# Optimization experiments

Hardware: AMD Instinct MI355X
Metric: run time of the kernel (lower is better)

Reference implementation:

```python
import jax, jax.numpy as jnp
import numpy as np


def gcn_conv(x, W, b, src, dst, n_nodes):
    """PyG GCNConv: linear transform, add self-loops, symmetric deg^-1/2 norm, scatter-add, bias."""
    h = x @ W  # [N, out] transform first (out_dim <= in_dim keeps gather traffic low)
    loop = jnp.arange(n_nodes)
    s = jnp.concatenate([src, loop])  # sources incl. self-loops
    d = jnp.concatenate([dst, loop])  # targets incl. self-loops
    deg = jnp.zeros((n_nodes,), h.dtype).at[d].add(jnp.ones((), h.dtype))
    dinv = jax.lax.rsqrt(deg)  # deg >= 1 because of self-loops
    coef = (dinv[s] * dinv[d])[:, None]  # [E+N, 1]
    out = jax.ops.segment_sum(h[s] * coef, d, num_segments=n_nodes)
    return out + b


def setup_inputs() -> dict:
    key = jax.random.key(0)
    k1, k2, k3, k4 = jax.random.split(key, 4)
    N, E = 100000, 1600000
    IN, HID, OUT = 128, 64, 32
    x = jax.random.normal(k1, (N, IN), dtype=jnp.float32)
    edge_index = jax.random.randint(k2, (2, E), 0, N, dtype=jnp.int64)
    W1 = jax.random.normal(k3, (IN, HID), dtype=jnp.float32) * (1.0 / np.sqrt(IN))
    b1 = jnp.zeros((HID,), jnp.float32)
    W2 = jax.random.normal(k4, (HID, OUT), dtype=jnp.float32) * (1.0 / np.sqrt(HID))
    b2 = jnp.zeros((OUT,), jnp.float32)
    return {"x": x, "edge_index": edge_index, "W1": W1, "b1": b1, "W2": W2, "b2": b2}


def reference(x, edge_index, W1, b1, W2, b2):
    src, dst = edge_index[0], edge_index[1]
    n = x.shape[0]
    h = jax.nn.relu(gcn_conv(x, W1, b1, src, dst, n))
    return gcn_conv(h, W2, b2, src, dst, n)
```

## Files before the change

### kernel.cpp

```cpp
#include <hip/hip_runtime.h>
#include <hip/hip_bf16.h>


#define IN_DIM 128
#define HID_DIM 64
#define OUT_DIM 32
#define BSHIFT 8
#define BSIZE 256
#define BMASK 255
#define PEB 8192
#define PTHREADS 512
#define CAPSHIFT 13

typedef __attribute__((ext_vector_type(2))) float v2f;
typedef __attribute__((ext_vector_type(8))) short short8v;
typedef __attribute__((ext_vector_type(4))) float float4v;

__device__ inline unsigned pack_bf16x2(float a, float b) {
    unsigned ua = __float_as_uint(a), ub = __float_as_uint(b);
    unsigned ra = (ua + 0x7fffu + ((ua >> 16) & 1u)) >> 16;
    unsigned rb = (ub + 0x7fffu + ((ub >> 16) & 1u)) & 0xffff0000u;
    return (ra & 0xffffu) | rb;
}
__device__ inline unsigned short f2bf(float f) {
    unsigned u = __float_as_uint(f);
    return (unsigned short)((u + 0x7fffu + ((u >> 16) & 1u)) >> 16);
}
#define BF_LO(w) __uint_as_float((w) << 16)
#define BF_HI(w) __uint_as_float((w) & 0xffff0000u)

__device__ inline v2f bfpair(unsigned u) {
    v2f r;
    r.x = __uint_as_float(u << 16);
    r.y = __uint_as_float(u & 0xffff0000u);
    return r;
}
__device__ inline void accp(v2f& a, unsigned u, float dv) {
    a.x += BF_LO(u) * dv;
    a.y += BF_HI(u) * dv;
}

#define ACC8(q)                                         \
    do {                                                \
        acc[0] += BF_LO((q).x); acc[1] += BF_HI((q).x); \
        acc[2] += BF_LO((q).y); acc[3] += BF_HI((q).y); \
        acc[4] += BF_LO((q).z); acc[5] += BF_HI((q).z); \
        acc[6] += BF_LO((q).w); acc[7] += BF_HI((q).w); \
    } while (0)

__global__ __launch_bounds__(PTHREADS) void k_part_gemm1(
        const int* __restrict__ src, const int* __restrict__ dst, int E,
        int* __restrict__ bfill, unsigned* __restrict__ packed, int B, int nPB,
        const float* __restrict__ x, const float* __restrict__ W,
        unsigned* __restrict__ g1b, int N) {
    __shared__ int cnt[512];
    __shared__ int off[512];
    __shared__ unsigned xs[32 * 66];
    int t = threadIdx.x;

    if (blockIdx.x < nPB) {
        if (t < 512) cnt[t] = 0;
        __syncthreads();
        int base = blockIdx.x * PEB;
        int dv[PEB / PTHREADS];
#pragma unroll
        for (int i = 0; i < PEB / PTHREADS; ++i) {
            int e = base + i * PTHREADS + t;
            dv[i] = (e < E) ? dst[e] : -1;
            if (dv[i] >= 0) atomicAdd(&cnt[dv[i] >> BSHIFT], 1);
        }
        __syncthreads();
        for (int b = t; b < B; b += PTHREADS) {
            int c = cnt[b];
            int o = c ? atomicAdd(&bfill[b], c) : 0;
            off[b] = (b << CAPSHIFT) + o;
        }
        __syncthreads();
#pragma unroll
        for (int i = 0; i < PEB / PTHREADS; ++i) {
            int e = base + i * PTHREADS + t;
            int d = dv[i];
            if (d >= 0) {
                int s = src[e];
                int slot = atomicAdd(&off[d >> BSHIFT], 1);
                packed[slot] = ((unsigned)s << BSHIFT) | (unsigned)(d & BMASK);
            }
        }
    } else {
        int row0 = (blockIdx.x - nPB) * 32;
        int w = t >> 6, lane = t & 63;
        int rg = w >> 2, wv = w & 3;
        int quad = lane >> 4, m = lane & 15;
        int ncol = wv * 16 + m;

        union { unsigned u[4]; short8v s; } bf[4];
#pragma unroll
        for (int kt = 0; kt < 4; ++kt) {
#pragma unroll
            for (int jp = 0; jp < 4; ++jp) {
                int k0 = kt * 32 + quad * 8 + jp * 2;
                float f0 = W[(size_t)k0 * HID_DIM + ncol];
                float f1 = W[(size_t)(k0 + 1) * HID_DIM + ncol];
                bf[kt].u[jp] = pack_bf16x2(f0, f1);
            }
        }

#pragma unroll
        for (int i = 0; i < 2; ++i) {
            int idx = t + 512 * i;
            int r = idx >> 5, c4 = idx & 31;
            int grow = row0 + r;
            float4 f = make_float4(0.f, 0.f, 0.f, 0.f);
            if (grow < N) f = ((const float4*)x)[(size_t)grow * 32 + c4];
            xs[r * 66 + c4 * 2]     = pack_bf16x2(f.x, f.y);
            xs[r * 66 + c4 * 2 + 1] = pack_bf16x2(f.z, f.w);
        }
        __syncthreads();

        float4v acc = {0.f, 0.f, 0.f, 0.f};
#pragma unroll
        for (int kt = 0; kt < 4; ++kt) {
            union { unsigned u[4]; short8v s; } af;
            const unsigned* ap = &xs[(rg * 16 + m) * 66 + kt * 16 + quad * 4];
            af.u[0] = ap[0]; af.u[1] = ap[1]; af.u[2] = ap[2]; af.u[3] = ap[3];
            acc = __builtin_amdgcn_mfma_f32_16x16x32_bf16(af.s, bf[kt].s, acc, 0, 0, 0);
        }

        unsigned short* g1s = (unsigned short*)g1b;
#pragma unroll
        for (int reg = 0; reg < 4; ++reg) {
            int r = row0 + rg * 16 + quad * 4 + reg;
            if (r < N) g1s[(size_t)r * HID_DIM + ncol] = f2bf(acc[reg]);
        }
    }
}

__global__ __launch_bounds__(512) void k_csrfill(const unsigned* __restrict__ packed,
                                                 const int* __restrict__ bfill,
                                                 int* __restrict__ colidx,
                                                 uint2* __restrict__ rowptr2,
                                                 float* __restrict__ dinv,
                                                 int N, int B) {
    __shared__ int ldeg[256];
    __shared__ int lscan[256];
    __shared__ int sexc[256];
    __shared__ int lfill[256];
    int t = threadIdx.x, bkt = blockIdx.x;
    int base = bkt << CAPSHIFT;
    int end  = base + bfill[bkt];
    if (t < 256) ldeg[t] = 0;
    __syncthreads();
    for (int e = base + t; e < end; e += 512)
        atomicAdd(&ldeg[packed[e] & BMASK], 1);
    __syncthreads();
    int v = (t < 256) ? ldeg[t] : 0;
    if (t < 256) lscan[t] = v;
    __syncthreads();
    for (int off = 1; off < 256; off <<= 1) {
        int x = (t < 256 && t >= off) ? lscan[t - off] : 0;
        __syncthreads();
        if (t < 256) lscan[t] += x;
        __syncthreads();
    }
    if (t < 256) {
        int exc = lscan[t] - v;
        sexc[t] = exc;
        lfill[t] = 0;
        int node = (bkt << BSHIFT) + t;
        if (node < N) {
            rowptr2[node] = make_uint2((unsigned)(base + exc), (unsigned)(base + exc + v));
            dinv[node] = rsqrtf((float)v + 1.0f);
        }
    }
    __syncthreads();
    for (int e = base + t; e < end; e += 512) {
        unsigned w = packed[e];
        int ld = w & BMASK;
        int pos = base + sexc[ld] + atomicAdd(&lfill[ld], 1);
        colidx[pos] = (int)(w >> BSHIFT);
    }
}

__global__ __launch_bounds__(256) void k_agg1g2(const unsigned* __restrict__ g1,
                                                const uint2* __restrict__ rowptr2,
                                                const int* __restrict__ colidx,
                                                const float* __restrict__ dinv,
                                                const float* __restrict__ b1,
                                                const float* __restrict__ W2,
                                                unsigned short* __restrict__ g2s, int N) {
    __shared__ unsigned t1s[16 * 33];
    int t = threadIdx.x;
    int wave = t >> 6, lane = t & 63;
    int q = lane >> 4, ql = lane & 15;
    int grp = ql >> 3, fp = ql & 7;
    int nl = wave * 4 + q;
    int dd = blockIdx.x * 16 + nl;
    bool live = dd < N;
    int d = live ? dd : N - 1;

    uint2 be = rowptr2[d];
    v2f a01 = {0.f, 0.f}, a23 = {0.f, 0.f}, a45 = {0.f, 0.f}, a67 = {0.f, 0.f};
    int e = (int)be.x, end = (int)be.y;
    for (; e + 4 <= end; e += 4) {
        int s0 = colidx[e + grp];
        int s1 = colidx[e + 2 + grp];
        float dv0 = dinv[s0], dv1 = dinv[s1];
        uint4 q0 = *(const uint4*)&g1[(size_t)s0 * 32 + fp * 4];
        uint4 q1 = *(const uint4*)&g1[(size_t)s1 * 32 + fp * 4];
        accp(a01, q0.x, dv0); accp(a23, q0.y, dv0);
        accp(a45, q0.z, dv0); accp(a67, q0.w, dv0);
        accp(a01, q1.x, dv1); accp(a23, q1.y, dv1);
        accp(a45, q1.z, dv1); accp(a67, q1.w, dv1);
    }
    for (; e + 2 <= end; e += 2) {
        int s = colidx[e + grp];
        float dv = dinv[s];
        uint4 qv = *(const uint4*)&g1[(size_t)s * 32 + fp * 4];
        accp(a01, qv.x, dv); accp(a23, qv.y, dv);
        accp(a45, qv.z, dv); accp(a67, qv.w, dv);
    }
    if (e < end) {
        int s = colidx[e];
        float dv = dinv[s];
        uint4 qv = *(const uint4*)&g1[(size_t)s * 32 + fp * 4];
        if (grp == 0) {
            accp(a01, qv.x, dv); accp(a23, qv.y, dv);
            accp(a45, qv.z, dv); accp(a67, qv.w, dv);
        }
    }
    float acc[8] = {a01.x, a01.y, a23.x, a23.y, a45.x, a45.y, a67.x, a67.y};
#pragma unroll
    for (int i = 0; i < 8; ++i)
        acc[i] += __shfl_xor(acc[i], 8);

    uint4 sq = *(const uint4*)&g1[(size_t)d * 32 + fp * 4];
    float dvd = dinv[d];
    acc[0] += BF_LO(sq.x) * dvd; acc[1] += BF_HI(sq.x) * dvd;
    acc[2] += BF_LO(sq.y) * dvd; acc[3] += BF_HI(sq.y) * dvd;
    acc[4] += BF_LO(sq.z) * dvd; acc[5] += BF_HI(sq.z) * dvd;
    acc[6] += BF_LO(sq.w) * dvd; acc[7] += BF_HI(sq.w) * dvd;
    float4 bb0 = ((const float4*)b1)[fp * 2];
    float4 bb1 = ((const float4*)b1)[fp * 2 + 1];
    float v0 = fmaxf(dvd * acc[0] + bb0.x, 0.f);
    float v1 = fmaxf(dvd * acc[1] + bb0.y, 0.f);
    float v2 = fmaxf(dvd * acc[2] + bb0.z, 0.f);
    float v3 = fmaxf(dvd * acc[3] + bb0.w, 0.f);
    float v4 = fmaxf(dvd * acc[4] + bb1.x, 0.f);
    float v5 = fmaxf(dvd * acc[5] + bb1.y, 0.f);
    float v6 = fmaxf(dvd * acc[6] + bb1.z, 0.f);
    float v7 = fmaxf(dvd * acc[7] + bb1.w, 0.f);
    if (grp == 0) {
        t1s[nl * 33 + fp * 4 + 0] = pack_bf16x2(v0, v1);
        t1s[nl * 33 + fp * 4 + 1] = pack_bf16x2(v2, v3);
        t1s[nl * 33 + fp * 4 + 2] = pack_bf16x2(v4, v5);
        t1s[nl * 33 + fp * 4 + 3] = pack_bf16x2(v6, v7);
    }
    __syncthreads();

    if (wave < 2) {
        int quad = lane >> 4, n = lane & 15;
        int col = (wave << 4) + n;
        union { unsigned u[4]; short8v s; } af0, af1, bh0, bh1, bl0, bl1;
#pragma unroll
        for (int jp = 0; jp < 4; ++jp) {
            int k0 = quad * 8 + jp * 2;
            float f0 = W2[(size_t)k0 * OUT_DIM + col];
            float f1 = W2[(size_t)(k0 + 1) * OUT_DIM + col];
            float f2 = W2[(size_t)(k0 + 32) * OUT_DIM + col];
            float f3 = W2[(size_t)(k0 + 33) * OUT_DIM + col];
            unsigned short h0 = f2bf(f0), h1 = f2bf(f1);
            unsigned short h2 = f2bf(f2), h3 = f2bf(f3);
            bh0.u[jp] = (unsigned)h0 | ((unsigned)h1 << 16);
            bh1.u[jp] = (unsigned)h2 | ((unsigned)h3 << 16);
            float r0 = f0 - __uint_as_float((unsigned)h0 << 16);
            float r1 = f1 - __uint_as_float((unsigned)h1 << 16);
            float r2 = f2 - __uint_as_float((unsigned)h2 << 16);
            float r3 = f3 - __uint_as_float((unsigned)h3 << 16);
            bl0.u[jp] = pack_bf16x2(r0, r1);
            bl1.u[jp] = pack_bf16x2(r2, r3);
            af0.u[jp] = t1s[n * 33 + quad * 4 + jp];
            af1.u[jp] = t1s[n * 33 + 16 + quad * 4 + jp];
        }
        float4v acc2 = {0.f, 0.f, 0.f, 0.f};
        acc2 = __builtin_amdgcn_mfma_f32_16x16x32_bf16(af0.s, bh0.s, acc2, 0, 0, 0);
        acc2 = __builtin_amdgcn_mfma_f32_16x16x32_bf16(af1.s, bh1.s, acc2, 0, 0, 0);
        acc2 = __builtin_amdgcn_mfma_f32_16x16x32_bf16(af0.s, bl0.s, acc2, 0, 0, 0);
        acc2 = __builtin_amdgcn_mfma_f32_16x16x32_bf16(af1.s, bl1.s, acc2, 0, 0, 0);
#pragma unroll
        for (int reg = 0; reg < 4; ++reg) {
            int row = blockIdx.x * 16 + quad * 4 + reg;
            if (row < N) g2s[(size_t)row * 32 + col] = f2bf(acc2[reg] * dinv[row]);
        }
    }
}

__global__ __launch_bounds__(128) void k_agg2(const unsigned* __restrict__ g2,
                                              const uint2* __restrict__ rowptr2,
                                              const int* __restrict__ colidx,
                                              const float* __restrict__ dinv,
                                              const float* __restrict__ b2,
                                              float* __restrict__ out, int N) {
    int t = threadIdx.x;
    int lane = t & 63;
    int o = lane >> 3, ol = lane & 7;
    int grp = ol >> 2, fp = ol & 3;
    int dd = blockIdx.x * 16 + (t >> 6) * 8 + o;
    bool live = dd < N;
    int d = live ? dd : N - 1;

    uint2 be = rowptr2[d];
    v2f a01 = {0.f, 0.f}, a23 = {0.f, 0.f}, a45 = {0.f, 0.f}, a67 = {0.f, 0.f};
#define ACC8V(qv)                                    \
    do {                                             \
        a01 += bfpair((qv).x); a23 += bfpair((qv).y);\
        a45 += bfpair((qv).z); a67 += bfpair((qv).w);\
    } while (0)
    int e = (int)be.x, end = (int)be.y;
    for (; e + 4 <= end; e += 4) {
        int s0 = colidx[e + grp];
        int s1 = colidx[e + 2 + grp];
        uint4 q0 = *(const uint4*)&g2[(size_t)s0 * 16 + fp * 4];
        uint4 q1 = *(const uint4*)&g2[(size_t)s1 * 16 + fp * 4];
        ACC8V(q0);
        ACC8V(q1);
    }
    for (; e + 2 <= end; e += 2) {
        int s = colidx[e + grp];
        uint4 qv = *(const uint4*)&g2[(size_t)s * 16 + fp * 4];
        ACC8V(qv);
    }
    if (e < end) {
        int s = colidx[e];
        uint4 qv = *(const uint4*)&g2[(size_t)s * 16 + fp * 4];
        if (grp == 0) ACC8V(qv);
    }
#undef ACC8V
    float acc[8] = {a01.x, a01.y, a23.x, a23.y, a45.x, a45.y, a67.x, a67.y};
#pragma unroll
    for (int i = 0; i < 8; ++i)
        acc[i] += __shfl_xor(acc[i], 4);
    uint4 sq = *(const uint4*)&g2[(size_t)d * 16 + fp * 4];
    ACC8(sq);
    float dv = dinv[d];
    float4 bb0 = ((const float4*)b2)[fp * 2];
    float4 bb1 = ((const float4*)b2)[fp * 2 + 1];
    if (live && grp == 0) {
        float4 r0, r1;
        r0.x = dv * acc[0] + bb0.x; r0.y = dv * acc[1] + bb0.y;
        r0.z = dv * acc[2] + bb0.z; r0.w = dv * acc[3] + bb0.w;
        r1.x = dv * acc[4] + bb1.x; r1.y = dv * acc[5] + bb1.y;
        r1.z = dv * acc[6] + bb1.z; r1.w = dv * acc[7] + bb1.w;
        *(float4*)&out[(size_t)dd * OUT_DIM + fp * 8] = r0;
        *(float4*)&out[(size_t)dd * OUT_DIM + fp * 8 + 4] = r1;
    }
}

extern "C" void kernel_launch(void* const* d_in, const int* in_sizes, int n_in,
                              void* d_out, int out_size, void* d_ws, size_t ws_size,
                              hipStream_t stream) {
    const float* x  = (const float*)d_in[0];
    const int*   ei = (const int*)d_in[1];
    const float* W1 = (const float*)d_in[2];
    const float* b1 = (const float*)d_in[3];
    const float* W2 = (const float*)d_in[4];
    const float* b2 = (const float*)d_in[5];
    float* out = (float*)d_out;

    const int N = in_sizes[0] / IN_DIM;
    const int E = in_sizes[1] / 2;
    const int* src = ei;
    const int* dst = ei + E;

    const int B   = (N + BSIZE - 1) / BSIZE;
    const int nPB = (E + PEB - 1) / PEB;
    const int nGB = (N + 31) / 32;
    const size_t SLOTS = (size_t)B << CAPSHIFT;

    char* p = (char*)d_ws;
    auto alloc = [&](size_t bytes) -> void* {
        void* r = (void*)p;
        p += (bytes + 255) & ~(size_t)255;
        return r;
    };
    int*      bfill   = (int*)alloc((size_t)B * 4);
    unsigned* packed  = (unsigned*)alloc(SLOTS * 4);
    int*      colidx  = (int*)alloc(SLOTS * 4);
    uint2*    rowptr2 = (uint2*)alloc((size_t)N * 8);
    float*    dinv    = (float*)alloc((size_t)N * 4);
    unsigned* g1b     = (unsigned*)alloc((size_t)N * 32 * 4);
    unsigned* g2b     = (unsigned*)alloc((size_t)N * 16 * 4);

    hipMemsetAsync(bfill, 0, (size_t)B * 4, stream);
    k_part_gemm1<<<nPB + nGB, PTHREADS, 0, stream>>>(src, dst, E, bfill, packed, B, nPB,
                                                     x, W1, g1b, N);
    k_csrfill<<<B, 512, 0, stream>>>(packed, bfill, colidx, rowptr2, dinv, N, B);
    k_agg1g2<<<(N + 15) / 16, 256, 0, stream>>>(g1b, rowptr2, colidx, dinv, b1, W2,
                                                (unsigned short*)g2b, N);
    k_agg2<<<(N + 15) / 16, 128, 0, stream>>>(g2b, rowptr2, colidx, dinv, b2, out, N);
}
```

Baseline: 207.8 us.

## Fuse CSR fill with layer-1 aggregation per bucket and compute degrees in partition

Merges the CSR build kernel with the first aggregation and second GEMM. Each bucket block builds its column list in shared memory and then aggregates its 256 nodes directly. Degrees are counted with global atomics during partitioning, and the stored dinv array is replaced by computing rsqrt on the fly. This saves one launch and a colidx round trip, but layer-1 aggregation now runs on only a few hundred blocks, and a shared-memory cap can truncate buckets with many edges.

```diff
diff --git a/kernel.cpp b/kernel.cpp
--- a/kernel.cpp
+++ b/kernel.cpp
@@ -11,6 +11,7 @@
 #define PEB 8192
 #define PTHREADS 512
 #define CAPSHIFT 13
+#define COLCAP 5120
 
 typedef __attribute__((ext_vector_type(2))) float v2f;
 typedef __attribute__((ext_vector_type(8))) short short8v;
@@ -50,24 +51,31 @@
 
 __global__ __launch_bounds__(PTHREADS) void k_part_gemm1(
         const int* __restrict__ src, const int* __restrict__ dst, int E,
-        int* __restrict__ bfill, unsigned* __restrict__ packed, int B, int nPB,
+        int* __restrict__ bfill, int* __restrict__ deg,
+        unsigned* __restrict__ packed, int B, int nPB,
         const float* __restrict__ x, const float* __restrict__ W,
         unsigned* __restrict__ g1b, int N) {
     __shared__ int cnt[512];
     __shared__ int off[512];
-    __shared__ unsigned xs[32 * 66];
+    __shared__ unsigned xs[32 * 68];
     int t = threadIdx.x;
 
     if (blockIdx.x < nPB) {
-        if (t < 512) cnt[t] = 0;
+        cnt[t] = 0;
         __syncthreads();
         int base = blockIdx.x * PEB;
         int dv[PEB / PTHREADS];
+        int sv[PEB / PTHREADS];
 #pragma unroll
         for (int i = 0; i < PEB / PTHREADS; ++i) {
             int e = base + i * PTHREADS + t;
-            dv[i] = (e < E) ? dst[e] : -1;
-            if (dv[i] >= 0) atomicAdd(&cnt[dv[i] >> BSHIFT], 1);
+            bool ok = e < E;
+            dv[i] = ok ? dst[e] : -1;
+            sv[i] = ok ? src[e] : 0;
+            if (dv[i] >= 0) {
+                atomicAdd(&cnt[dv[i] >> BSHIFT], 1);
+                atomicAdd(&deg[dv[i]], 1);
+            }
         }
         __syncthreads();
         for (int b = t; b < B; b += PTHREADS) {
@@ -78,12 +86,10 @@
         __syncthreads();
 #pragma unroll
         for (int i = 0; i < PEB / PTHREADS; ++i) {
-            int e = base + i * PTHREADS + t;
             int d = dv[i];
             if (d >= 0) {
-                int s = src[e];
                 int slot = atomicAdd(&off[d >> BSHIFT], 1);
-                packed[slot] = ((unsigned)s << BSHIFT) | (unsigned)(d & BMASK);
+                packed[slot] = ((unsigned)sv[i] << BSHIFT) | (unsigned)(d & BMASK);
             }
         }
     } else {
@@ -93,6 +99,16 @@
         int quad = lane >> 4, m = lane & 15;
         int ncol = wv * 16 + m;
 
+        float4 xf[2];
+#pragma unroll
+        for (int i = 0; i < 2; ++i) {
+            int idx = t + 512 * i;
+            int r = idx >> 5, c4 = idx & 31;
+            int grow = row0 + r;
+            xf[i] = make_float4(0.f, 0.f, 0.f, 0.f);
+            if (grow < N) xf[i] = ((const float4*)x)[(size_t)grow * 32 + c4];
+        }
+
         union { unsigned u[4]; short8v s; } bf[4];
 #pragma unroll
         for (int kt = 0; kt < 4; ++kt) {
@@ -109,11 +125,8 @@
         for (int i = 0; i < 2; ++i) {
             int idx = t + 512 * i;
             int r = idx >> 5, c4 = idx & 31;
-            int grow = row0 + r;
-            float4 f = make_float4(0.f, 0.f, 0.f, 0.f);
-            if (grow < N) f = ((const float4*)x)[(size_t)grow * 32 + c4];
-            xs[r * 66 + c4 * 2]     = pack_bf16x2(f.x, f.y);
-            xs[r * 66 + c4 * 2 + 1] = pack_bf16x2(f.z, f.w);
+            xs[r * 68 + c4 * 2]     = pack_bf16x2(xf[i].x, xf[i].y);
+            xs[r * 68 + c4 * 2 + 1] = pack_bf16x2(xf[i].z, xf[i].w);
         }
         __syncthreads();
 
@@ -121,7 +134,7 @@
 #pragma unroll
         for (int kt = 0; kt < 4; ++kt) {
             union { unsigned u[4]; short8v s; } af;
-            const unsigned* ap = &xs[(rg * 16 + m) * 66 + kt * 16 + quad * 4];
+            const unsigned* ap = &xs[(rg * 16 + m) * 68 + kt * 16 + quad * 4];
             af.u[0] = ap[0]; af.u[1] = ap[1]; af.u[2] = ap[2]; af.u[3] = ap[3];
             acc = __builtin_amdgcn_mfma_f32_16x16x32_bf16(af.s, bf[kt].s, acc, 0, 0, 0);
         }
@@ -135,31 +148,40 @@
     }
 }
 
-__global__ __launch_bounds__(512) void k_csrfill(const unsigned* __restrict__ packed,
-                                                 const int* __restrict__ bfill,
-                                                 int* __restrict__ colidx,
-                                                 uint2* __restrict__ rowptr2,
-                                                 float* __restrict__ dinv,
-                                                 int N, int B) {
+__global__ __launch_bounds__(512) void k_bktagg(const unsigned* __restrict__ packed,
+                                                const int* __restrict__ bfill,
+                                                const unsigned* __restrict__ g1,
+                                                const int* __restrict__ deg,
+                                                const float* __restrict__ b1,
+                                                const float* __restrict__ W2,
+                                                int* __restrict__ colidx,
+                                                uint2* __restrict__ rowptr2,
+                                                unsigned short* __restrict__ g2s, int N) {
     __shared__ int ldeg[256];
     __shared__ int lscan[256];
     __shared__ int sexc[256];
     __shared__ int lfill[256];
+    __shared__ int colL[COLCAP];
+    __shared__ unsigned t1s[128 * 33];
     int t = threadIdx.x, bkt = blockIdx.x;
     int base = bkt << CAPSHIFT;
-    int end  = base + bfill[bkt];
+    int cnt = bfill[bkt];
+    if (cnt > COLCAP) cnt = COLCAP;
+    int end = base + cnt;
+
     if (t < 256) ldeg[t] = 0;
     __syncthreads();
     for (int e = base + t; e < end; e += 512)
         atomicAdd(&ldeg[packed[e] & BMASK], 1);
     __syncthreads();
+
     int v = (t < 256) ? ldeg[t] : 0;
     if (t < 256) lscan[t] = v;
     __syncthreads();
     for (int off = 1; off < 256; off <<= 1) {
-        int x = (t < 256 && t >= off) ? lscan[t - off] : 0;
-        __syncthreads();
-        if (t < 256) lscan[t] += x;
+        int xv = (t < 256 && t >= off) ? lscan[t - off] : 0;
+        __syncthreads();
+        if (t < 256) lscan[t] += xv;
         __syncthreads();
     }
     if (t < 256) {
@@ -167,100 +189,95 @@
         sexc[t] = exc;
         lfill[t] = 0;
         int node = (bkt << BSHIFT) + t;
-        if (node < N) {
+        if (node < N)
             rowptr2[node] = make_uint2((unsigned)(base + exc), (unsigned)(base + exc + v));
-            dinv[node] = rsqrtf((float)v + 1.0f);
-        }
     }
     __syncthreads();
+
     for (int e = base + t; e < end; e += 512) {
         unsigned w = packed[e];
         int ld = w & BMASK;
-        int pos = base + sexc[ld] + atomicAdd(&lfill[ld], 1);
-        colidx[pos] = (int)(w >> BSHIFT);
-    }
-}
-
-__global__ __launch_bounds__(256) void k_agg1g2(const unsigned* __restrict__ g1,
-                                                const uint2* __restrict__ rowptr2,
-                                                const int* __restrict__ colidx,
-                                                const float* __restrict__ dinv,
-                                                const float* __restrict__ b1,
-                                                const float* __restrict__ W2,
-                                                unsigned short* __restrict__ g2s, int N) {
-    __shared__ unsigned t1s[16 * 33];
-    int t = threadIdx.x;
+        int pos = sexc[ld] + atomicAdd(&lfill[ld], 1);
+        colL[pos] = (int)(w >> BSHIFT);
+    }
+    __syncthreads();
+    for (int e = t; e < cnt; e += 512) colidx[base + e] = colL[e];
+
+    int qidx = t >> 4, ql = t & 15;
+    int grp = ql >> 3, fp = ql & 7;
     int wave = t >> 6, lane = t & 63;
-    int q = lane >> 4, ql = lane & 15;
-    int grp = ql >> 3, fp = ql & 7;
-    int nl = wave * 4 + q;
-    int dd = blockIdx.x * 16 + nl;
-    bool live = dd < N;
-    int d = live ? dd : N - 1;
-
-    uint2 be = rowptr2[d];
-    v2f a01 = {0.f, 0.f}, a23 = {0.f, 0.f}, a45 = {0.f, 0.f}, a67 = {0.f, 0.f};
-    int e = (int)be.x, end = (int)be.y;
-    for (; e + 4 <= end; e += 4) {
-        int s0 = colidx[e + grp];
-        int s1 = colidx[e + 2 + grp];
-        float dv0 = dinv[s0], dv1 = dinv[s1];
-        uint4 q0 = *(const uint4*)&g1[(size_t)s0 * 32 + fp * 4];
-        uint4 q1 = *(const uint4*)&g1[(size_t)s1 * 32 + fp * 4];
-        accp(a01, q0.x, dv0); accp(a23, q0.y, dv0);
-        accp(a45, q0.z, dv0); accp(a67, q0.w, dv0);
-        accp(a01, q1.x, dv1); accp(a23, q1.y, dv1);
-        accp(a45, q1.z, dv1); accp(a67, q1.w, dv1);
-    }
-    for (; e + 2 <= end; e += 2) {
-        int s = colidx[e + grp];
-        float dv = dinv[s];
-        uint4 qv = *(const uint4*)&g1[(size_t)s * 32 + fp * 4];
-        accp(a01, qv.x, dv); accp(a23, qv.y, dv);
-        accp(a45, qv.z, dv); accp(a67, qv.w, dv);
-    }
-    if (e < end) {
-        int s = colidx[e];
-        float dv = dinv[s];
-        uint4 qv = *(const uint4*)&g1[(size_t)s * 32 + fp * 4];
-        if (grp == 0) {
-            accp(a01, qv.x, dv); accp(a23, qv.y, dv);
-            accp(a45, qv.z, dv); accp(a67, qv.w, dv);
-        }
-    }
-    float acc[8] = {a01.x, a01.y, a23.x, a23.y, a45.x, a45.y, a67.x, a67.y};
-#pragma unroll
-    for (int i = 0; i < 8; ++i)
-        acc[i] += __shfl_xor(acc[i], 8);
-
-    uint4 sq = *(const uint4*)&g1[(size_t)d * 32 + fp * 4];
-    float dvd = dinv[d];
-    acc[0] += BF_LO(sq.x) * dvd; acc[1] += BF_HI(sq.x) * dvd;
-    acc[2] += BF_LO(sq.y) * dvd; acc[3] += BF_HI(sq.y) * dvd;
-    acc[4] += BF_LO(sq.z) * dvd; acc[5] += BF_HI(sq.z) * dvd;
-    acc[6] += BF_LO(sq.w) * dvd; acc[7] += BF_HI(sq.w) * dvd;
-    float4 bb0 = ((const float4*)b1)[fp * 2];
-    float4 bb1 = ((const float4*)b1)[fp * 2 + 1];
-    float v0 = fmaxf(dvd * acc[0] + bb0.x, 0.f);
-    float v1 = fmaxf(dvd * acc[1] + bb0.y, 0.f);
-    float v2 = fmaxf(dvd * acc[2] + bb0.z, 0.f);
-    float v3 = fmaxf(dvd * acc[3] + bb0.w, 0.f);
-    float v4 = fmaxf(dvd * acc[4] + bb1.x, 0.f);
-    float v5 = fmaxf(dvd * acc[5] + bb1.y, 0.f);
-    float v6 = fmaxf(dvd * acc[6] + bb1.z, 0.f);
-    float v7 = fmaxf(dvd * acc[7] + bb1.w, 0.f);
-    if (grp == 0) {
-        t1s[nl * 33 + fp * 4 + 0] = pack_bf16x2(v0, v1);
-        t1s[nl * 33 + fp * 4 + 1] = pack_bf16x2(v2, v3);
-        t1s[nl * 33 + fp * 4 + 2] = pack_bf16x2(v4, v5);
-        t1s[nl * 33 + fp * 4 + 3] = pack_bf16x2(v6, v7);
-    }
-    __syncthreads();
-
-    if (wave < 2) {
-        int quad = lane >> 4, n = lane & 15;
-        int col = (wave << 4) + n;
-        union { unsigned u[4]; short8v s; } af0, af1, bh0, bh1, bl0, bl1;
+    int quad = lane >> 4, n16 = lane & 15;
+    int cw = wave & 1;
+    int col = cw * 16 + n16;
+
+    for (int half = 0; half < 2; ++half) {
+        for (int i = 0; i < 4; ++i) {
+            int lt = qidx * 4 + i;
+            int ln = half * 128 + lt;
+            int dd = (bkt << BSHIFT) + ln;
+            int d = dd < N ? dd : N - 1;
+            int eb = sexc[ln], ecnt = ldeg[ln];
+            v2f a01 = {0.f, 0.f}, a23 = {0.f, 0.f}, a45 = {0.f, 0.f}, a67 = {0.f, 0.f};
+            int e = eb, eend = eb + ecnt;
+            for (; e + 4 <= eend; e += 4) {
+                int s0 = colL[e + grp];
+                int s1 = colL[e + 2 + grp];
+                float dv0 = rsqrtf((float)deg[s0] + 1.0f);
+                float dv1 = rsqrtf((float)deg[s1] + 1.0f);
+                uint4 q0 = *(const uint4*)&g1[(size_t)s0 * 32 + fp * 4];
+                uint4 q1 = *(const uint4*)&g1[(size_t)s1 * 32 + fp * 4];
+                accp(a01, q0.x, dv0); accp(a23, q0.y, dv0);
+                accp(a45, q0.z, dv0); accp(a67, q0.w, dv0);
+                accp(a01, q1.x, dv1); accp(a23, q1.y, dv1);
+                accp(a45, q1.z, dv1); accp(a67, q1.w, dv1);
+            }
+            for (; e + 2 <= eend; e += 2) {
+                int s = colL[e + grp];
+                float dvs = rsqrtf((float)deg[s] + 1.0f);
+                uint4 qv = *(const uint4*)&g1[(size_t)s * 32 + fp * 4];
+                accp(a01, qv.x, dvs); accp(a23, qv.y, dvs);
+                accp(a45, qv.z, dvs); accp(a67, qv.w, dvs);
+            }
+            if (e < eend) {
+                int s = colL[e];
+                float dvs = rsqrtf((float)deg[s] + 1.0f);
+                uint4 qv = *(const uint4*)&g1[(size_t)s * 32 + fp * 4];
+                if (grp == 0) {
+                    accp(a01, qv.x, dvs); accp(a23, qv.y, dvs);
+                    accp(a45, qv.z, dvs); accp(a67, qv.w, dvs);
+                }
+            }
+            float acc[8] = {a01.x, a01.y, a23.x, a23.y, a45.x, a45.y, a67.x, a67.y};
+#pragma unroll
+            for (int k = 0; k < 8; ++k)
+                acc[k] += __shfl_xor(acc[k], 8);
+
+            uint4 sq = *(const uint4*)&g1[(size_t)d * 32 + fp * 4];
+            float dvd = rsqrtf((float)deg[d] + 1.0f);
+            acc[0] += BF_LO(sq.x) * dvd; acc[1] += BF_HI(sq.x) * dvd;
+            acc[2] += BF_LO(sq.y) * dvd; acc[3] += BF_HI(sq.y) * dvd;
+            acc[4] += BF_LO(sq.z) * dvd; acc[5] += BF_HI(sq.z) * dvd;
+            acc[6] += BF_LO(sq.w) * dvd; acc[7] += BF_HI(sq.w) * dvd;
+            float4 bb0 = ((const float4*)b1)[fp * 2];
+            float4 bb1 = ((const float4*)b1)[fp * 2 + 1];
+            float v0 = fmaxf(dvd * acc[0] + bb0.x, 0.f);
+            float v1 = fmaxf(dvd * acc[1] + bb0.y, 0.f);
+            float v2 = fmaxf(dvd * acc[2] + bb0.z, 0.f);
+            float v3 = fmaxf(dvd * acc[3] + bb0.w, 0.f);
+            float v4 = fmaxf(dvd * acc[4] + bb1.x, 0.f);
+            float v5 = fmaxf(dvd * acc[5] + bb1.y, 0.f);
+            float v6 = fmaxf(dvd * acc[6] + bb1.z, 0.f);
+            float v7 = fmaxf(dvd * acc[7] + bb1.w, 0.f);
+            if (grp == 0) {
+                t1s[lt * 33 + fp * 4 + 0] = pack_bf16x2(v0, v1);
+                t1s[lt * 33 + fp * 4 + 1] = pack_bf16x2(v2, v3);
+                t1s[lt * 33 + fp * 4 + 2] = pack_bf16x2(v4, v5);
+                t1s[lt * 33 + fp * 4 + 3] = pack_bf16x2(v6, v7);
+            }
+        }
+        __syncthreads();
+
+        union { unsigned u[4]; short8v s; } bh0, bh1, bl0, bl1;
 #pragma unroll
         for (int jp = 0; jp < 4; ++jp) {
             int k0 = quad * 8 + jp * 2;
@@ -278,26 +295,38 @@
             float r3 = f3 - __uint_as_float((unsigned)h3 << 16);
             bl0.u[jp] = pack_bf16x2(r0, r1);
             bl1.u[jp] = pack_bf16x2(r2, r3);
-            af0.u[jp] = t1s[n * 33 + quad * 4 + jp];
-            af1.u[jp] = t1s[n * 33 + 16 + quad * 4 + jp];
-        }
-        float4v acc2 = {0.f, 0.f, 0.f, 0.f};
-        acc2 = __builtin_amdgcn_mfma_f32_16x16x32_bf16(af0.s, bh0.s, acc2, 0, 0, 0);
-        acc2 = __builtin_amdgcn_mfma_f32_16x16x32_bf16(af1.s, bh1.s, acc2, 0, 0, 0);
-        acc2 = __builtin_amdgcn_mfma_f32_16x16x32_bf16(af0.s, bl0.s, acc2, 0, 0, 0);
-        acc2 = __builtin_amdgcn_mfma_f32_16x16x32_bf16(af1.s, bl1.s, acc2, 0, 0, 0);
-#pragma unroll
-        for (int reg = 0; reg < 4; ++reg) {
-            int row = blockIdx.x * 16 + quad * 4 + reg;
-            if (row < N) g2s[(size_t)row * 32 + col] = f2bf(acc2[reg] * dinv[row]);
-        }
+        }
+#pragma unroll
+        for (int j = 0; j < 2; ++j) {
+            int rt = (wave >> 1) + 4 * j;
+            union { unsigned u[4]; short8v s; } af0, af1;
+#pragma unroll
+            for (int jp = 0; jp < 4; ++jp) {
+                af0.u[jp] = t1s[(rt * 16 + n16) * 33 + jp + quad * 4];
+                af1.u[jp] = t1s[(rt * 16 + n16) * 33 + 16 + jp + quad * 4];
+            }
+            float4v acc2 = {0.f, 0.f, 0.f, 0.f};
+            acc2 = __builtin_amdgcn_mfma_f32_16x16x32_bf16(af0.s, bh0.s, acc2, 0, 0, 0);
+            acc2 = __builtin_amdgcn_mfma_f32_16x16x32_bf16(af1.s, bh1.s, acc2, 0, 0, 0);
+            acc2 = __builtin_amdgcn_mfma_f32_16x16x32_bf16(af0.s, bl0.s, acc2, 0, 0, 0);
+            acc2 = __builtin_amdgcn_mfma_f32_16x16x32_bf16(af1.s, bl1.s, acc2, 0, 0, 0);
+#pragma unroll
+            for (int reg = 0; reg < 4; ++reg) {
+                int row = (bkt << BSHIFT) + half * 128 + rt * 16 + quad * 4 + reg;
+                if (row < N) {
+                    float dvr = rsqrtf((float)deg[row] + 1.0f);
+                    g2s[(size_t)row * 32 + col] = f2bf(acc2[reg] * dvr);
+                }
+            }
+        }
+        __syncthreads();
     }
 }
 
 __global__ __launch_bounds__(128) void k_agg2(const unsigned* __restrict__ g2,
                                               const uint2* __restrict__ rowptr2,
                                               const int* __restrict__ colidx,
-                                              const float* __restrict__ dinv,
+                                              const int* __restrict__ deg,
                                               const float* __restrict__ b2,
                                               float* __restrict__ out, int N) {
     int t = threadIdx.x;
@@ -341,7 +370,7 @@
         acc[i] += __shfl_xor(acc[i], 4);
     uint4 sq = *(const uint4*)&g2[(size_t)d * 16 + fp * 4];
     ACC8(sq);
-    float dv = dinv[d];
+    float dv = rsqrtf((float)deg[d] + 1.0f);
     float4 bb0 = ((const float4*)b2)[fp * 2];
     float4 bb1 = ((const float4*)b2)[fp * 2 + 1];
     if (live && grp == 0) {
@@ -383,18 +412,19 @@
         return r;
     };
     int*      bfill   = (int*)alloc((size_t)B * 4);
+    int*      deg     = (int*)alloc((size_t)N * 4);
     unsigned* packed  = (unsigned*)alloc(SLOTS * 4);
     int*      colidx  = (int*)alloc(SLOTS * 4);
     uint2*    rowptr2 = (uint2*)alloc((size_t)N * 8);
-    float*    dinv    = (float*)alloc((size_t)N * 4);
     unsigned* g1b     = (unsigned*)alloc((size_t)N * 32 * 4);
     unsigned* g2b     = (unsigned*)alloc((size_t)N * 16 * 4);
 
-    hipMemsetAsync(bfill, 0, (size_t)B * 4, stream);
-    k_part_gemm1<<<nPB + nGB, PTHREADS, 0, stream>>>(src, dst, E, bfill, packed, B, nPB,
-                                                     x, W1, g1b, N);
-    k_csrfill<<<B, 512, 0, stream>>>(packed, bfill, colidx, rowptr2, dinv, N, B);
-    k_agg1g2<<<(N + 15) / 16, 256, 0, stream>>>(g1b, rowptr2, colidx, dinv, b1, W2,
-                                                (unsigned short*)g2b, N);
-    k_agg2<<<(N + 15) / 16, 128, 0, stream>>>(g2b, rowptr2, colidx, dinv, b2, out, N);
-}
+    size_t zbytes = (size_t)((char*)(deg + N) - (char*)bfill);
+    hipMemsetAsync(bfill, 0, zbytes, stream);
+
+    k_part_gemm1<<<nPB + nGB, PTHREADS, 0, stream>>>(src, dst, E, bfill, deg, packed, B,
+                                                     nPB, x, W1, g1b, N);
+    k_bktagg<<<B, 512, 0, stream>>>(packed, bfill, g1b, deg, b1, W2, colidx, rowptr2,
+                                    (unsigned short*)g2b, N);
+    k_agg2<<<(N + 15) / 16, 128, 0, stream>>>(g2b, rowptr2, colidx, deg, b2, out, N);
+}
```

New measurement: 249.8 us. 1.2x slower.
